# Performance work log

Hardware: AMD Instinct MI355X
Metric: run time of the kernel (lower is better)

## Reference

```python
import jax, jax.numpy as jnp
import numpy as np

B, C, H = 2, 256, 64
INTER = 64


def setup_inputs() -> dict:
    key = jax.random.key(0)
    ks = jax.random.split(key, 10)
    scale = 1.0 / np.sqrt(C)
    x = jax.random.normal(ks[0], (B, C, H, H), dtype=jnp.float32)
    # binary hole mask (1 = foreground/hole region)
    mask = jnp.round(jax.random.uniform(ks[1], (B, 1, H, H), dtype=jnp.float32))
    def w(k, shape, s):
        return jax.random.normal(k, shape, dtype=jnp.float32) * s
    return {
        "x": x,
        "mask": mask,
        "w_theta_s": w(ks[2], (INTER, C), scale),
        "w_phi_s": w(ks[3], (INTER, C), scale),
        "w_gate_s": w(ks[4], (INTER, C), scale),
        "w_theta_c": w(ks[5], (INTER, C), scale),
        "w_phi_c": w(ks[6], (INTER, C), scale),
        "w_gate_c": w(ks[7], (INTER, C), scale),
        "w_out": w(ks[8], (C, INTER), 1.0 / np.sqrt(INTER)),
    }


def _nonlocal_branch(q_src, kv_src, w_theta, w_phi, w_gate):
    # q_src, kv_src: [B, C, N]; weights: [inter, C]
    K = jnp.einsum('oc,bcn->bon', w_theta, kv_src)   # [B, inter, N]
    Q = jnp.einsum('oc,bcn->bon', w_phi, q_src)      # [B, inter, N]
    score = jnp.einsum('bom,bon->bmn', Q, K)         # [B, Nq, Nk]
    score = jax.nn.softmax(score, axis=-1)
    V = jnp.einsum('oc,bcn->bon', w_gate, kv_src)    # [B, inter, N]
    feat = jnp.einsum('bon,bmn->bom', V, score)      # [B, inter, Nq]
    return feat, score


def reference(x, mask, w_theta_s, w_phi_s, w_gate_s,
              w_theta_c, w_phi_c, w_gate_c, w_out):
    b, c, h = x.shape[0], x.shape[1], x.shape[2]
    n = h * h
    fg = (x * mask).reshape(b, c, n)          # foreground tokens
    bg = (x * (1.0 - mask)).reshape(b, c, n)  # background tokens
    feat_self, score_self = _nonlocal_branch(fg, fg, w_theta_s, w_phi_s, w_gate_s)
    feat_cross, score_cross = _nonlocal_branch(fg, bg, w_theta_c, w_phi_c, w_gate_c)
    fused = jnp.einsum('co,bon->bcn', w_out, feat_self + feat_cross)
    feat = x + fused.reshape(b, c, h, h)
    return feat, score_self, score_cross
```

## Files before the change

### kernel.cpp

```cpp
#include <hip/hip_runtime.h>
#include <hip/hip_bf16.h>
#include <stdint.h>

#define NBATCH 2
#define NCH    256
#define NTOK   4096
#define NINT   64
#define CHW    64
#define QCOLS  1024
#define NCHQ   (QCOLS/CHW)

typedef float  f32x4  __attribute__((ext_vector_type(4)));
typedef __bf16 bf16x8 __attribute__((ext_vector_type(8)));
union U16x8 { uint4 u; bf16x8 b; };

#define SZBF      ((size_t)NTOK*NINT)
#define RL_OFF_B  ((size_t)4194304)

#define OUT_SELF  ((size_t)2097152)
#define OUT_CROSS ((size_t)35651584)
#define FPART_OFF_F (OUT_SELF)
#define LPART_OFF_F (OUT_SELF + (size_t)4194304)

__device__ inline unsigned short f2bf(float x){
  unsigned int u = __builtin_bit_cast(unsigned int, x);
  u = (u + 0x7FFFu + ((u>>16)&1u)) >> 16;
  return (unsigned short)u;
}
__device__ inline float bf2f(unsigned short s){
  unsigned int u = ((unsigned int)s)<<16;
  return __builtin_bit_cast(float, u);
}

typedef __attribute__((address_space(3))) unsigned int lds_u32_t;
typedef __attribute__((address_space(1))) const unsigned int gbl_u32_t;
__device__ inline void async16(const void* g, void* l){
  __builtin_amdgcn_global_load_lds((gbl_u32_t*)g, (lds_u32_t*)l, 16, 0, 0);
}
__device__ inline void wgbar(){
  asm volatile("" ::: "memory");
  __builtin_amdgcn_s_barrier();
  asm volatile("" ::: "memory");
}

__global__ __launch_bounds__(256) void k_proj(
    const float* __restrict__ x, const float* __restrict__ mask,
    const float* __restrict__ wts, const float* __restrict__ wps,
    const float* __restrict__ wgs, const float* __restrict__ wtc,
    const float* __restrict__ wpc, const float* __restrict__ wgc,
    char* __restrict__ ws)
{
  int nt = blockIdx.x;
  int j  = blockIdx.y;
  int b  = blockIdx.z;
  const float* W; int isBg, mode, arrH, arrL;
  switch (j) {
    case 0: W=wts; isBg=0; mode=0; arrH=2; arrL=3; break;
    case 1: W=wps; isBg=0; mode=0; arrH=0; arrL=1; break;
    case 2: W=wgs; isBg=0; mode=1; arrH=8; arrL=8; break;
    case 3: W=wpc; isBg=0; mode=0; arrH=4; arrL=5; break;
    case 4: W=wtc; isBg=1; mode=0; arrH=6; arrL=7; break;
    default:W=wgc; isBg=1; mode=1; arrH=9; arrL=9; break;
  }
  __shared__ float xm[256*64];
  __shared__ float msk[64];
  int t = threadIdx.x;
  if (t < 64) {
    float m = mask[(size_t)b*NTOK + nt*64 + t];
    msk[t] = isBg ? (1.0f - m) : m;
  }
  __syncthreads();
  const float* xb = x + (size_t)b*NCH*NTOK + nt*64;
  for (int it = 0; it < 64; ++it) {
    int flat = it*256 + t; int c = flat>>6, nl = flat&63;
    xm[flat] = xb[(size_t)c*NTOK + nl] * msk[nl];
  }
  __syncthreads();
  int nl = t & 63;
  int o0 = __builtin_amdgcn_readfirstlane((t>>6)*16);
  const float* Wr = W + (size_t)o0*256;
  float acc[16];
  #pragma unroll
  for (int i=0;i<16;i++) acc[i]=0.0f;
  #pragma unroll 4
  for (int c=0;c<256;c++){
    float xv = xm[c*64+nl];
    #pragma unroll
    for (int i=0;i<16;i++) acc[i] += Wr[i*256 + c] * xv;
  }
  int n = nt*64 + nl;
  if (mode==0){
    unsigned short* Ah = (unsigned short*)ws + ((size_t)b*10 + arrH)*SZBF;
    unsigned short* Al = (unsigned short*)ws + ((size_t)b*10 + arrL)*SZBF;
    #pragma unroll
    for (int i=0;i<16;i++){
      float v = acc[i];
      unsigned short h = f2bf(v);
      float r = v - bf2f(h);
      Ah[(size_t)n*NINT + o0+i] = h;
      Al[(size_t)n*NINT + o0+i] = f2bf(r);
    }
  } else {
    unsigned short* V = (unsigned short*)ws + ((size_t)b*10 + arrH)*SZBF;
    #pragma unroll
    for (int i=0;i<16;i++) V[(size_t)(o0+i)*NTOK + n] = f2bf(acc[i]);
  }
}

__global__ __launch_bounds__(256) void k_s1(char* __restrict__ ws, float* __restrict__ out)
{
  __shared__ __align__(16) char smem[40960];

  int blk = blockIdx.x;
  int xcd = blk & 7, idx = blk >> 3;
  int bbr = xcd >> 1;
  int unit = ((xcd & 1) << 7) | idx;
  int qtr = unit & 3, mb = unit >> 2;
  int b = bbr >> 1, br = bbr & 1;
  const unsigned short* Qh = (const unsigned short*)ws + ((size_t)b*10 + (br?4:0))*SZBF;
  const unsigned short* Ql = Qh + SZBF;
  const unsigned short* Kh = (const unsigned short*)ws + ((size_t)b*10 + (br?6:2))*SZBF;
  const unsigned short* Kl = Kh + SZBF;
  const unsigned short* Vv = (const unsigned short*)ws + ((size_t)b*10 + (br?9:8))*SZBF;

  int t = threadIdx.x, lane = t&63, w = t>>6;
  int rowb = lane&15, q4 = lane>>4, ko = q4*8;
  int m0 = mb*64 + w*16, mrow = m0 + rowb;

  unsigned short* lPw = (unsigned short*)(smem + 32768 + w*2048);

  U16x8 qh[2], ql[2];
  #pragma unroll
  for (int kk=0;kk<2;kk++){
    qh[kk].u = *(const uint4*)(Qh + (size_t)mrow*NINT + kk*32 + ko);
    ql[kk].u = *(const uint4*)(Ql + (size_t)mrow*NINT + kk*32 + ko);
  }

  auto lkbase = [&](int buf)->unsigned short*{
    return (unsigned short*)(smem + (size_t)buf*16384);
  };
  auto stage = [&](int ch, int buf){
    int n0 = qtr*QCOLS + ch*CHW;
    const unsigned short* gH = Kh + (size_t)n0*NINT;
    const unsigned short* gL = Kl + (size_t)n0*NINT;
    unsigned short* LB = lkbase(buf);
    #pragma unroll
    for (int it=0; it<2; ++it){
      int f = it*256 + t;
      int r = f>>3, g = f&7, gs = g ^ (r&7);
      size_t goff = (size_t)r*64 + gs*8;
      async16(gH + goff, LB + (size_t)f*8);
      async16(gL + goff, LB + 4096 + (size_t)f*8);
    }
  };

  f32x4 fac[4];
  #pragma unroll
  for (int ot=0;ot<4;ot++) fac[ot] = (f32x4){0.0f,0.0f,0.0f,0.0f};
  float Lacc = 0.0f;

  stage(0, 0);
  for (int ch=0; ch<NCHQ; ++ch){
    int cur = ch & 1;
    asm volatile("s_waitcnt vmcnt(0)" ::: "memory");
    wgbar();
    if (ch+1 < NCHQ) stage(ch+1, cur^1);
    asm volatile("" ::: "memory");
    __builtin_amdgcn_sched_barrier(0);
    unsigned short* LB = lkbase(cur);
    int n0 = qtr*QCOLS + ch*CHW;
    #pragma unroll
    for (int t8=0; t8<4; ++t8){
      int row = t8*16 + rowb;
      f32x4 s = {0.0f,0.0f,0.0f,0.0f};
      #pragma unroll
      for (int kk=0; kk<2; ++kk){
        int soff = row*64 + (((kk*4 + q4) ^ (row&7))*8);
        U16x8 ah, al;
        ah.u = *(const uint4*)(LB + soff);
        al.u = *(const uint4*)(LB + 4096 + soff);
        s = __builtin_amdgcn_mfma_f32_16x16x32_bf16(ah.b, qh[kk].b, s, 0,0,0);
        s = __builtin_amdgcn_mfma_f32_16x16x32_bf16(ah.b, ql[kk].b, s, 0,0,0);
        s = __builtin_amdgcn_mfma_f32_16x16x32_bf16(al.b, qh[kk].b, s, 0,0,0);
      }
      float p0=__expf(s[0]), p1=__expf(s[1]), p2=__expf(s[2]), p3=__expf(s[3]);
      Lacc += (p0+p1)+(p2+p3);
      unsigned int lo = (unsigned int)f2bf(p0) | ((unsigned int)f2bf(p1)<<16);
      unsigned int hi = (unsigned int)f2bf(p2) | ((unsigned int)f2bf(p3)<<16);
      uint2 pk; pk.x = lo; pk.y = hi;
      int g  = t8*2 + (q4>>1);
      int gs = g ^ (rowb&7);
      *(uint2*)(lPw + rowb*64 + gs*8 + (q4&1)*4) = pk;
    }
    asm volatile("s_waitcnt lgkmcnt(0)" ::: "memory");
    __builtin_amdgcn_sched_barrier(0);
    #pragma unroll
    for (int kk4=0; kk4<2; ++kk4){
      int rs = (kk4*4 + q4) ^ (rowb&7);
      U16x8 pa;
      pa.u = *(const uint4*)(lPw + rowb*64 + rs*8);
      #pragma unroll
      for (int ot=0; ot<4; ++ot){
        U16x8 vb;
        vb.u = *(const uint4*)(Vv + (size_t)(ot*16+rowb)*NTOK + n0 + kk4*32 + ko);
        fac[ot] = __builtin_amdgcn_mfma_f32_16x16x32_bf16(pa.b, vb.b, fac[ot], 0,0,0);
      }
    }
    asm volatile("s_waitcnt lgkmcnt(0)" ::: "memory");
  }

  #pragma unroll
  for (int d=16; d<64; d<<=1) Lacc += __shfl_xor(Lacc, d, 64);
  if (q4==0)
    out[LPART_OFF_F + (size_t)(bbr*4+qtr)*NTOK + m0 + rowb] = Lacc;

  float* FP = out + FPART_OFF_F + (size_t)(bbr*4+qtr)*NTOK*NINT;
  #pragma unroll
  for (int ot=0; ot<4; ++ot)
    #pragma unroll
    for (int r=0; r<4; ++r)
      FP[(size_t)(m0 + q4*4 + r)*NINT + ot*16 + rowb] = fac[ot][r];
}

__global__ __launch_bounds__(256) void k_rl(char* __restrict__ ws, const float* __restrict__ out)
{
  int idxg = blockIdx.x*256 + threadIdx.x;
  int bbr = idxg >> 12, row = idxg & 4095;
  const float* LP = out + LPART_OFF_F;
  float L = 0.0f;
  #pragma unroll
  for (int q=0;q<4;q++) L += LP[(size_t)(bbr*4+q)*NTOK + row];
  ((float*)(ws + RL_OFF_B))[(size_t)bbr*NTOK + row] = 1.0f / L;
}

__global__ __launch_bounds__(256) void k_epi(
    const float* __restrict__ x, const float* __restrict__ wout,
    const char* __restrict__ ws, float* __restrict__ out)
{
  int nt = blockIdx.x, b = blockIdx.y;
  int t = threadIdx.x, nl = t&63;
  const float* FP = out + FPART_OFF_F;
  const float* rL = (const float*)(ws + RL_OFF_B);
  __shared__ float fs[64][65];
  int b0 = b*2, b1 = b*2+1;
  for (int it=0; it<16; ++it){
    int flat = it*256 + t; int n_l = flat>>6, o = flat&63;
    int row = nt*64 + n_l;
    float s0=0.0f, s1=0.0f;
    #pragma unroll
    for (int q=0;q<4;q++){
      s0 += FP[((size_t)(b0*4+q)*NTOK + row)*NINT + o];
      s1 += FP[((size_t)(b1*4+q)*NTOK + row)*NINT + o];
    }
    fs[n_l][o] = s0*rL[(size_t)b0*NTOK+row] + s1*rL[(size_t)b1*NTOK+row];
  }
  __syncthreads();
  float f[64];
  #pragma unroll
  for (int o=0;o<64;o++) f[o] = fs[nl][o];
  int c0 = __builtin_amdgcn_readfirstlane((t>>6)*64);
  const float* wr = wout + (size_t)c0*64;
  for (int cc=0; cc<64; ++cc){
    int c = c0 + cc;
    float acc = x[((size_t)b*NCH + c)*NTOK + nt*64 + nl];
    #pragma unroll
    for (int o=0;o<64;o++) acc += wr[cc*64+o]*f[o];
    out[((size_t)b*NCH + c)*NTOK + nt*64 + nl] = acc;
  }
}

__global__ __launch_bounds__(256) void k_s2(const char* __restrict__ ws, float* __restrict__ out)
{
  __shared__ __align__(16) char smem[32768];

  int blk = blockIdx.x;
  int xcd = blk & 7, idx = blk >> 3;
  int bbr = xcd >> 1;
  int unit = ((xcd & 1) << 7) | idx;
  int qtr = unit & 3, mb = unit >> 2;
  int b = bbr >> 1, br = bbr & 1;
  const unsigned short* Qh = (const unsigned short*)ws + ((size_t)b*10 + (br?4:0))*SZBF;
  const unsigned short* Ql = Qh + SZBF;
  const unsigned short* Kh = (const unsigned short*)ws + ((size_t)b*10 + (br?6:2))*SZBF;
  const unsigned short* Kl = Kh + SZBF;

  int t = threadIdx.x, lane = t&63, w = t>>6;
  int rowb = lane&15, q4 = lane>>4, ko = q4*8;
  int m0 = mb*64 + w*16, mrow = m0 + rowb;

  float rLp = ((const float*)(ws + RL_OFF_B))[(size_t)bbr*NTOK + mrow];

  U16x8 qh[2], ql[2];
  #pragma unroll
  for (int kk=0;kk<2;kk++){
    qh[kk].u = *(const uint4*)(Qh + (size_t)mrow*NINT + kk*32 + ko);
    ql[kk].u = *(const uint4*)(Ql + (size_t)mrow*NINT + kk*32 + ko);
  }

  auto lkbase = [&](int buf)->unsigned short*{
    return (unsigned short*)(smem + (size_t)buf*16384);
  };
  auto stage = [&](int ch, int buf){
    int n0 = qtr*QCOLS + ch*CHW;
    const unsigned short* gH = Kh + (size_t)n0*NINT;
    const unsigned short* gL = Kl + (size_t)n0*NINT;
    unsigned short* LB = lkbase(buf);
    #pragma unroll
    for (int it=0; it<2; ++it){
      int f = it*256 + t;
      int r = f>>3, g = f&7, gs = g ^ (r&7);
      size_t goff = (size_t)r*64 + gs*8;
      async16(gH + goff, LB + (size_t)f*8);
      async16(gL + goff, LB + 4096 + (size_t)f*8);
    }
  };

  float* outS = out + (br ? OUT_CROSS : OUT_SELF) + (size_t)b*NTOK*NTOK;

  stage(0, 0);
  for (int ch=0; ch<NCHQ; ++ch){
    int cur = ch & 1;
    if (ch == 0) { asm volatile("s_waitcnt vmcnt(0)" ::: "memory"); }
    else         { asm volatile("s_waitcnt vmcnt(4)" ::: "memory"); }
    wgbar();
    if (ch+1 < NCHQ) stage(ch+1, cur^1);
    asm volatile("" ::: "memory");
    __builtin_amdgcn_sched_barrier(0);
    unsigned short* LB = lkbase(cur);
    int n0 = qtr*QCOLS + ch*CHW;
    #pragma unroll
    for (int t8=0; t8<4; ++t8){
      int row = t8*16 + rowb;
      f32x4 s = {0.0f,0.0f,0.0f,0.0f};
      #pragma unroll
      for (int kk=0; kk<2; ++kk){
        int soff = row*64 + (((kk*4 + q4) ^ (row&7))*8);
        U16x8 ah, al;
        ah.u = *(const uint4*)(LB + soff);
        al.u = *(const uint4*)(LB + 4096 + soff);
        s = __builtin_amdgcn_mfma_f32_16x16x32_bf16(ah.b, qh[kk].b, s, 0,0,0);
        s = __builtin_amdgcn_mfma_f32_16x16x32_bf16(ah.b, ql[kk].b, s, 0,0,0);
        s = __builtin_amdgcn_mfma_f32_16x16x32_bf16(al.b, qh[kk].b, s, 0,0,0);
      }
      f32x4 p;
      p[0] = __expf(s[0])*rLp; p[1] = __expf(s[1])*rLp;
      p[2] = __expf(s[2])*rLp; p[3] = __expf(s[3])*rLp;
      __builtin_nontemporal_store(p,
          (f32x4*)(outS + (size_t)mrow*NTOK + n0 + t8*16 + q4*4));
    }
  }
}

extern "C" void kernel_launch(void* const* d_in, const int* in_sizes, int n_in,
                              void* d_out, int out_size, void* d_ws, size_t ws_size,
                              hipStream_t stream)
{
  const float* x    = (const float*)d_in[0];
  const float* mask = (const float*)d_in[1];
  const float* wts  = (const float*)d_in[2];
  const float* wps  = (const float*)d_in[3];
  const float* wgs  = (const float*)d_in[4];
  const float* wtc  = (const float*)d_in[5];
  const float* wpc  = (const float*)d_in[6];
  const float* wgc  = (const float*)d_in[7];
  const float* wout = (const float*)d_in[8];
  float* out = (float*)d_out;
  char*  ws  = (char*)d_ws;
  (void)in_sizes; (void)n_in; (void)out_size; (void)ws_size;

  k_proj <<<dim3(64,6,NBATCH), 256, 0, stream>>>(x, mask, wts, wps, wgs, wtc, wpc, wgc, ws);
  k_s1   <<<dim3(1024), 256, 0, stream>>>(ws, out);
  k_rl   <<<dim3(64),   256, 0, stream>>>(ws, out);
  k_epi  <<<dim3(64,NBATCH), 256, 0, stream>>>(x, wout, ws, out);
  k_s2   <<<dim3(1024), 256, 0, stream>>>(ws, out);
}
```

Measured before the change: 555.6 us.

## Drop LDS staging of K in score kernels, fuse row-sum inversion into epilogue

The score kernels k_s1 and k_s2 no longer stage K tiles into LDS through async global-to-LDS copies with double buffering. They load the K fragments straight from global memory into registers and add an occupancy hint of 4 blocks per SM. The k_rl kernel is folded into k_epi, which now computes the reciprocal row sums itself and uses smaller 32-token tiles over twice as many blocks. k_proj splits its channel loop into two halves to halve shared memory. Together these aim to raise occupancy and cut one launch, at the cost of less explicit overlap between memory traffic and compute and more redundant global reads of K.

```diff
diff --git a/kernel.cpp b/kernel.cpp
--- a/kernel.cpp
+++ b/kernel.cpp
@@ -30,17 +30,6 @@
 __device__ inline float bf2f(unsigned short s){
   unsigned int u = ((unsigned int)s)<<16;
   return __builtin_bit_cast(float, u);
-}
-
-typedef __attribute__((address_space(3))) unsigned int lds_u32_t;
-typedef __attribute__((address_space(1))) const unsigned int gbl_u32_t;
-__device__ inline void async16(const void* g, void* l){
-  __builtin_amdgcn_global_load_lds((gbl_u32_t*)g, (lds_u32_t*)l, 16, 0, 0);
-}
-__device__ inline void wgbar(){
-  asm volatile("" ::: "memory");
-  __builtin_amdgcn_s_barrier();
-  asm volatile("" ::: "memory");
 }
 
 __global__ __launch_bounds__(256) void k_proj(
@@ -62,7 +51,7 @@
     case 4: W=wtc; isBg=1; mode=0; arrH=6; arrL=7; break;
     default:W=wgc; isBg=1; mode=1; arrH=9; arrL=9; break;
   }
-  __shared__ float xm[256*64];
+  __shared__ float xm[128*64];
   __shared__ float msk[64];
   int t = threadIdx.x;
   if (t < 64) {
@@ -71,22 +60,27 @@
   }
   __syncthreads();
   const float* xb = x + (size_t)b*NCH*NTOK + nt*64;
-  for (int it = 0; it < 64; ++it) {
-    int flat = it*256 + t; int c = flat>>6, nl = flat&63;
-    xm[flat] = xb[(size_t)c*NTOK + nl] * msk[nl];
-  }
-  __syncthreads();
   int nl = t & 63;
   int o0 = __builtin_amdgcn_readfirstlane((t>>6)*16);
   const float* Wr = W + (size_t)o0*256;
   float acc[16];
   #pragma unroll
   for (int i=0;i<16;i++) acc[i]=0.0f;
-  #pragma unroll 4
-  for (int c=0;c<256;c++){
-    float xv = xm[c*64+nl];
-    #pragma unroll
-    for (int i=0;i<16;i++) acc[i] += Wr[i*256 + c] * xv;
+  for (int p=0; p<2; ++p){
+    const float* xbp = xb + (size_t)p*128*NTOK;
+    for (int it = 0; it < 32; ++it) {
+      int flat = it*256 + t; int c = flat>>6, n2 = flat&63;
+      xm[flat] = xbp[(size_t)c*NTOK + n2] * msk[n2];
+    }
+    __syncthreads();
+    #pragma unroll 4
+    for (int cc=0;cc<128;cc++){
+      int c = p*128 + cc;
+      float xv = xm[cc*64+nl];
+      #pragma unroll
+      for (int i=0;i<16;i++) acc[i] += Wr[i*256 + c] * xv;
+    }
+    __syncthreads();
   }
   int n = nt*64 + nl;
   if (mode==0){
@@ -107,9 +101,9 @@
   }
 }
 
-__global__ __launch_bounds__(256) void k_s1(char* __restrict__ ws, float* __restrict__ out)
-{
-  __shared__ __align__(16) char smem[40960];
+__global__ __launch_bounds__(256,4) void k_s1(char* __restrict__ ws, float* __restrict__ out)
+{
+  __shared__ __align__(16) unsigned short lP[4][1024];
 
   int blk = blockIdx.x;
   int xcd = blk & 7, idx = blk >> 3;
@@ -127,7 +121,7 @@
   int rowb = lane&15, q4 = lane>>4, ko = q4*8;
   int m0 = mb*64 + w*16, mrow = m0 + rowb;
 
-  unsigned short* lPw = (unsigned short*)(smem + 32768 + w*2048);
+  unsigned short* lPw = lP[w];
 
   U16x8 qh[2], ql[2];
   #pragma unroll
@@ -136,49 +130,24 @@
     ql[kk].u = *(const uint4*)(Ql + (size_t)mrow*NINT + kk*32 + ko);
   }
 
-  auto lkbase = [&](int buf)->unsigned short*{
-    return (unsigned short*)(smem + (size_t)buf*16384);
-  };
-  auto stage = [&](int ch, int buf){
-    int n0 = qtr*QCOLS + ch*CHW;
-    const unsigned short* gH = Kh + (size_t)n0*NINT;
-    const unsigned short* gL = Kl + (size_t)n0*NINT;
-    unsigned short* LB = lkbase(buf);
-    #pragma unroll
-    for (int it=0; it<2; ++it){
-      int f = it*256 + t;
-      int r = f>>3, g = f&7, gs = g ^ (r&7);
-      size_t goff = (size_t)r*64 + gs*8;
-      async16(gH + goff, LB + (size_t)f*8);
-      async16(gL + goff, LB + 4096 + (size_t)f*8);
-    }
-  };
-
   f32x4 fac[4];
   #pragma unroll
   for (int ot=0;ot<4;ot++) fac[ot] = (f32x4){0.0f,0.0f,0.0f,0.0f};
   float Lacc = 0.0f;
 
-  stage(0, 0);
   for (int ch=0; ch<NCHQ; ++ch){
-    int cur = ch & 1;
-    asm volatile("s_waitcnt vmcnt(0)" ::: "memory");
-    wgbar();
-    if (ch+1 < NCHQ) stage(ch+1, cur^1);
-    asm volatile("" ::: "memory");
-    __builtin_amdgcn_sched_barrier(0);
-    unsigned short* LB = lkbase(cur);
     int n0 = qtr*QCOLS + ch*CHW;
     #pragma unroll
     for (int t8=0; t8<4; ++t8){
-      int row = t8*16 + rowb;
+      int row = n0 + t8*16 + rowb;
+      const unsigned short* krh = Kh + (size_t)row*NINT;
+      const unsigned short* krl = Kl + (size_t)row*NINT;
       f32x4 s = {0.0f,0.0f,0.0f,0.0f};
       #pragma unroll
       for (int kk=0; kk<2; ++kk){
-        int soff = row*64 + (((kk*4 + q4) ^ (row&7))*8);
         U16x8 ah, al;
-        ah.u = *(const uint4*)(LB + soff);
-        al.u = *(const uint4*)(LB + 4096 + soff);
+        ah.u = *(const uint4*)(krh + kk*32 + ko);
+        al.u = *(const uint4*)(krl + kk*32 + ko);
         s = __builtin_amdgcn_mfma_f32_16x16x32_bf16(ah.b, qh[kk].b, s, 0,0,0);
         s = __builtin_amdgcn_mfma_f32_16x16x32_bf16(ah.b, ql[kk].b, s, 0,0,0);
         s = __builtin_amdgcn_mfma_f32_16x16x32_bf16(al.b, qh[kk].b, s, 0,0,0);
@@ -192,8 +161,6 @@
       int gs = g ^ (rowb&7);
       *(uint2*)(lPw + rowb*64 + gs*8 + (q4&1)*4) = pk;
     }
-    asm volatile("s_waitcnt lgkmcnt(0)" ::: "memory");
-    __builtin_amdgcn_sched_barrier(0);
     #pragma unroll
     for (int kk4=0; kk4<2; ++kk4){
       int rs = (kk4*4 + q4) ^ (rowb&7);
@@ -206,7 +173,6 @@
         fac[ot] = __builtin_amdgcn_mfma_f32_16x16x32_bf16(pa.b, vb.b, fac[ot], 0,0,0);
       }
     }
-    asm volatile("s_waitcnt lgkmcnt(0)" ::: "memory");
   }
 
   #pragma unroll
@@ -222,57 +188,59 @@
       FP[(size_t)(m0 + q4*4 + r)*NINT + ot*16 + rowb] = fac[ot][r];
 }
 
-__global__ __launch_bounds__(256) void k_rl(char* __restrict__ ws, const float* __restrict__ out)
-{
-  int idxg = blockIdx.x*256 + threadIdx.x;
-  int bbr = idxg >> 12, row = idxg & 4095;
-  const float* LP = out + LPART_OFF_F;
-  float L = 0.0f;
-  #pragma unroll
-  for (int q=0;q<4;q++) L += LP[(size_t)(bbr*4+q)*NTOK + row];
-  ((float*)(ws + RL_OFF_B))[(size_t)bbr*NTOK + row] = 1.0f / L;
-}
-
 __global__ __launch_bounds__(256) void k_epi(
     const float* __restrict__ x, const float* __restrict__ wout,
-    const char* __restrict__ ws, float* __restrict__ out)
+    char* __restrict__ ws, float* __restrict__ out)
 {
   int nt = blockIdx.x, b = blockIdx.y;
-  int t = threadIdx.x, nl = t&63;
+  int t = threadIdx.x;
   const float* FP = out + FPART_OFF_F;
-  const float* rL = (const float*)(ws + RL_OFF_B);
-  __shared__ float fs[64][65];
+  const float* LP = out + LPART_OFF_F;
+  float* rL = (float*)(ws + RL_OFF_B);
+  __shared__ float fs[32][65];
+  __shared__ float rls[2][32];
   int b0 = b*2, b1 = b*2+1;
-  for (int it=0; it<16; ++it){
+  if (t < 64){
+    int hb = t>>5, rloc = t&31;
+    int bb = b*2 + hb;
+    int row = nt*32 + rloc;
+    float L = 0.0f;
+    #pragma unroll
+    for (int q=0;q<4;q++) L += LP[(size_t)(bb*4+q)*NTOK + row];
+    float r = 1.0f / L;
+    rls[hb][rloc] = r;
+    rL[(size_t)bb*NTOK + row] = r;
+  }
+  __syncthreads();
+  for (int it=0; it<8; ++it){
     int flat = it*256 + t; int n_l = flat>>6, o = flat&63;
-    int row = nt*64 + n_l;
+    int row = nt*32 + n_l;
     float s0=0.0f, s1=0.0f;
     #pragma unroll
     for (int q=0;q<4;q++){
       s0 += FP[((size_t)(b0*4+q)*NTOK + row)*NINT + o];
       s1 += FP[((size_t)(b1*4+q)*NTOK + row)*NINT + o];
     }
-    fs[n_l][o] = s0*rL[(size_t)b0*NTOK+row] + s1*rL[(size_t)b1*NTOK+row];
+    fs[n_l][o] = s0*rls[0][n_l] + s1*rls[1][n_l];
   }
   __syncthreads();
+  int nl = t&31, cg = t>>5, c0 = cg*32;
   float f[64];
   #pragma unroll
   for (int o=0;o<64;o++) f[o] = fs[nl][o];
-  int c0 = __builtin_amdgcn_readfirstlane((t>>6)*64);
   const float* wr = wout + (size_t)c0*64;
-  for (int cc=0; cc<64; ++cc){
+  int row = nt*32 + nl;
+  for (int cc=0; cc<32; ++cc){
     int c = c0 + cc;
-    float acc = x[((size_t)b*NCH + c)*NTOK + nt*64 + nl];
+    float acc = x[((size_t)b*NCH + c)*NTOK + row];
     #pragma unroll
     for (int o=0;o<64;o++) acc += wr[cc*64+o]*f[o];
-    out[((size_t)b*NCH + c)*NTOK + nt*64 + nl] = acc;
-  }
-}
-
-__global__ __launch_bounds__(256) void k_s2(const char* __restrict__ ws, float* __restrict__ out)
-{
-  __shared__ __align__(16) char smem[32768];
-
+    out[((size_t)b*NCH + c)*NTOK + row] = acc;
+  }
+}
+
+__global__ __launch_bounds__(256,4) void k_s2(const char* __restrict__ ws, float* __restrict__ out)
+{
   int blk = blockIdx.x;
   int xcd = blk & 7, idx = blk >> 3;
   int bbr = xcd >> 1;
@@ -297,47 +265,21 @@
     ql[kk].u = *(const uint4*)(Ql + (size_t)mrow*NINT + kk*32 + ko);
   }
 
-  auto lkbase = [&](int buf)->unsigned short*{
-    return (unsigned short*)(smem + (size_t)buf*16384);
-  };
-  auto stage = [&](int ch, int buf){
+  float* outS = out + (br ? OUT_CROSS : OUT_SELF) + (size_t)b*NTOK*NTOK;
+
+  for (int ch=0; ch<NCHQ; ++ch){
     int n0 = qtr*QCOLS + ch*CHW;
-    const unsigned short* gH = Kh + (size_t)n0*NINT;
-    const unsigned short* gL = Kl + (size_t)n0*NINT;
-    unsigned short* LB = lkbase(buf);
-    #pragma unroll
-    for (int it=0; it<2; ++it){
-      int f = it*256 + t;
-      int r = f>>3, g = f&7, gs = g ^ (r&7);
-      size_t goff = (size_t)r*64 + gs*8;
-      async16(gH + goff, LB + (size_t)f*8);
-      async16(gL + goff, LB + 4096 + (size_t)f*8);
-    }
-  };
-
-  float* outS = out + (br ? OUT_CROSS : OUT_SELF) + (size_t)b*NTOK*NTOK;
-
-  stage(0, 0);
-  for (int ch=0; ch<NCHQ; ++ch){
-    int cur = ch & 1;
-    if (ch == 0) { asm volatile("s_waitcnt vmcnt(0)" ::: "memory"); }
-    else         { asm volatile("s_waitcnt vmcnt(4)" ::: "memory"); }
-    wgbar();
-    if (ch+1 < NCHQ) stage(ch+1, cur^1);
-    asm volatile("" ::: "memory");
-    __builtin_amdgcn_sched_barrier(0);
-    unsigned short* LB = lkbase(cur);
-    int n0 = qtr*QCOLS + ch*CHW;
     #pragma unroll
     for (int t8=0; t8<4; ++t8){
-      int row = t8*16 + rowb;
+      int row = n0 + t8*16 + rowb;
+      const unsigned short* krh = Kh + (size_t)row*NINT;
+      const unsigned short* krl = Kl + (size_t)row*NINT;
       f32x4 s = {0.0f,0.0f,0.0f,0.0f};
       #pragma unroll
       for (int kk=0; kk<2; ++kk){
-        int soff = row*64 + (((kk*4 + q4) ^ (row&7))*8);
         U16x8 ah, al;
-        ah.u = *(const uint4*)(LB + soff);
-        al.u = *(const uint4*)(LB + 4096 + soff);
+        ah.u = *(const uint4*)(krh + kk*32 + ko);
+        al.u = *(const uint4*)(krl + kk*32 + ko);
         s = __builtin_amdgcn_mfma_f32_16x16x32_bf16(ah.b, qh[kk].b, s, 0,0,0);
         s = __builtin_amdgcn_mfma_f32_16x16x32_bf16(ah.b, ql[kk].b, s, 0,0,0);
         s = __builtin_amdgcn_mfma_f32_16x16x32_bf16(al.b, qh[kk].b, s, 0,0,0);
@@ -370,7 +312,6 @@
 
   k_proj <<<dim3(64,6,NBATCH), 256, 0, stream>>>(x, mask, wts, wps, wgs, wtc, wpc, wgc, ws);
   k_s1   <<<dim3(1024), 256, 0, stream>>>(ws, out);
-  k_rl   <<<dim3(64),   256, 0, stream>>>(ws, out);
-  k_epi  <<<dim3(64,NBATCH), 256, 0, stream>>>(x, wout, ws, out);
+  k_epi  <<<dim3(128,NBATCH), 256, 0, stream>>>(x, wout, ws, out);
   k_s2   <<<dim3(1024), 256, 0, stream>>>(ws, out);
 }
```

New measurement: 618.5 us. 1.11x slower.
